# Performance work log

Measured on AMD Instinct MI355X. Metric: run time of the kernel, lower is better.

Reference implementation:

```python
import jax, jax.numpy as jnp
import numpy as np

K = 16      # n_sample neighbors
L = 2       # stacked PT blocks
D = 128     # in_dim
H = 128     # hidden_dim = out_dim = vector_dim
EPS = 1e-5


def _bn(x, g, b, axes):
    # batch-norm with batch statistics (train-mode MinkowskiBatchNorm / BN1d / BN2d)
    m = jnp.mean(x, axes, keepdims=True)
    v = jnp.var(x, axes, keepdims=True)
    return (x - m) * jax.lax.rsqrt(v + EPS) * g + b


def setup_inputs():
    key = jax.random.key(0)
    ks = jax.random.split(key, 16)
    B, Nper = 2, 8192
    coords = jax.random.randint(ks[0], (B, Nper, 3), 0, 200, dtype=jnp.int32)
    feats = jax.random.normal(ks[1], (B * Nper, D), dtype=jnp.float32)
    w = lambda k, s: jax.random.normal(k, s, dtype=jnp.float32) * 0.1
    return {
        'coords': coords, 'feats': feats,
        'W_top': w(ks[2], (L, D, H)),
        'bn_top_g': jnp.ones((L, H)), 'bn_top_b': jnp.zeros((L, H)),
        'W_phi': w(ks[3], (L, H, H)),
        'W_psi': w(ks[4], (L, H, H)),
        'W_alpha': w(ks[5], (L, H, H)),
        'W_d1': w(ks[6], (L, 3, H)), 'b_d1': jnp.zeros((L, H)),
        'bn_d1_g': jnp.ones((L, H)), 'bn_d1_b': jnp.zeros((L, H)),
        'W_d2': w(ks[7], (L, H, H)), 'b_d2': jnp.zeros((L, H)),
        'bn_d2_g': jnp.ones((L, H)), 'bn_d2_b': jnp.zeros((L, H)),
        'W_g1': w(ks[8], (L, H, H)), 'b_g1': jnp.zeros((L, H)),
        'bn_g1_g': jnp.ones((L, H)), 'bn_g1_b': jnp.zeros((L, H)),
        'W_g2': w(ks[9], (L, H, H)), 'b_g2': jnp.zeros((L, H)),
        'bn_g2_g': jnp.ones((L, H)), 'bn_g2_b': jnp.zeros((L, H)),
        'W_down': w(ks[10], (L, H, D)),
        'bn_down_g': jnp.ones((L, D)), 'bn_down_b': jnp.zeros((L, D)),
    }


def _knn(coords):
    # cube_query with USE_KNN=True: per-scene KNN grouping (self included)
    cf = coords.astype(jnp.float32)

    def one(c):  # c: (Nper, 3)
        d2 = jnp.sum((c[:, None, :] - c[None, :, :]) ** 2, -1)  # (Nper, Nper)
        _, idx = jax.lax.top_k(-d2, K)
        return idx

    idx = jax.vmap(one)(cf)                      # (B, Nper, K) per-scene indices
    nbr = jax.vmap(lambda c, i: c[i])(cf, idx)   # (B, Nper, K, 3) grouped coords
    rel = nbr - cf[:, :, None, :]                # relative xyz (pose input)
    B, Nper = coords.shape[0], coords.shape[1]
    gidx = (idx + (jnp.arange(B, dtype=idx.dtype) * Nper)[:, None, None]).reshape(-1, K)
    return rel.reshape(-1, K, 3), gidx           # (N,K,3), (N,K) global indices


def reference(coords, feats, W_top, bn_top_g, bn_top_b, W_phi, W_psi, W_alpha,
              W_d1, b_d1, bn_d1_g, bn_d1_b, W_d2, b_d2, bn_d2_g, bn_d2_b,
              W_g1, b_g1, bn_g1_g, bn_g1_b, W_g2, b_g2, bn_g2_g, bn_g2_b,
              W_down, bn_down_g, bn_down_b):
    rel, gidx = _knn(coords)
    f = feats
    for l in range(L):
        h = _bn(f @ W_top[l], bn_top_g[l], bn_top_b[l], 0)  # linear_top (1x1 conv + BN)
        # delta: pointwise MLP 3 -> H -> H on relative xyz (position encoding)
        pose = jax.nn.relu(_bn(rel @ W_d1[l] + b_d1[l], bn_d1_g[l], bn_d1_b[l], (0, 1)))
        pose = _bn(pose @ W_d2[l] + b_d2[l], bn_d2_g[l], bn_d2_b[l], (0, 1))  # (N,K,H)
        q = h @ W_phi[l]               # (N, H)
        kk = (h @ W_psi[l])[gidx]      # neighbor keys   (N, K, H)
        v = (h @ W_alpha[l])[gidx]     # neighbor values (N, K, H)
        # gamma: pointwise MLP on (phi - psi + pose), vector attention logits
        a = q[:, None, :] - kk + pose
        a = jax.nn.relu(_bn(a @ W_g1[l] + b_g1[l], bn_g1_g[l], bn_g1_b[l], (0, 1)))
        a = _bn(a @ W_g2[l] + b_g2[l], bn_g2_g[l], bn_g2_b[l], (0, 1))
        attn = jax.nn.softmax(a, axis=1)          # per-channel softmax over K neighbors
        y = jnp.sum(attn * (v + pose), axis=1)    # (N, H) vector-attention aggregation
        y = _bn(y @ W_down[l], bn_down_g[l], bn_down_b[l], 0)  # linear_down + BN
        f = y + f                                  # residual
    return f
```

## Files before the change

### kernel.cpp

```cpp
#include <hip/hip_runtime.h>

using u16 = unsigned short;
using u32 = unsigned int;
using u64 = unsigned long long;

#define NPTS   16384
#define NPER   8192
#define KNN    16
#define NKROWS (NPTS*KNN)
#define HD     128
#define CAP    208
#define NSLOT  16
#define NREG   10

typedef _Float16 half8 __attribute__((ext_vector_type(8)));
typedef float    floatx4 __attribute__((ext_vector_type(4)));
typedef short          s16x2 __attribute__((ext_vector_type(2)));
typedef unsigned short u16x2 __attribute__((ext_vector_type(2)));
typedef _Float16       h2v   __attribute__((ext_vector_type(2)));

__device__ __forceinline__ u16  f2h(float f){ _Float16 h=(_Float16)f; return __builtin_bit_cast(u16,h); }
__device__ __forceinline__ float h2f(u16 u){ return (float)__builtin_bit_cast(_Float16,u); }
__device__ __forceinline__ u32 umin32(u32 a,u32 b){ return a<b?a:b; }
__device__ __forceinline__ u32 mbcnt64(u64 m){
    return __builtin_amdgcn_mbcnt_hi((u32)(m>>32), __builtin_amdgcn_mbcnt_lo((u32)m,0));
}
__device__ __forceinline__ h2v bch2(u32 x){ return __builtin_bit_cast(h2v,x); }
__device__ __forceinline__ u32 bcu(h2v x){ return __builtin_bit_cast(u32,x); }
__device__ __forceinline__ u32 pk_relu(u32 x){
    u32 r;
    asm("v_pk_max_f16 %0, %1, %2" : "=v"(r) : "v"(x), "v"(0u));
    return r;
}
__device__ __forceinline__ int sdot2_acc(s16x2 a, int c){
#if __has_builtin(__builtin_amdgcn_sdot2)
    return __builtin_amdgcn_sdot2(a, a, c, false);
#else
    return (int)a.x*(int)a.x + (int)a.y*(int)a.y + c;
#endif
}

__global__ __launch_bounds__(256) void pack_coords(const int* __restrict__ coords, u32* __restrict__ pc){
    int i = blockIdx.x*256 + threadIdx.x;
    pc[i] = (u32)coords[3*i] | ((u32)coords[3*i+1]<<8) | ((u32)coords[3*i+2]<<16);
}

struct WPtrs { const float* p[8]; };
__global__ __launch_bounds__(256) void prep_weights(WPtrs wp, u16* __restrict__ wt){
    int idx = blockIdx.x*256 + threadIdx.x;
    int t = idx>>15, rem = idx&32767;
    int l = rem>>14, e = rem&16383;
    int n = e>>7, k = e&127;
    wt[idx] = f2h(wp.p[t][l*16384 + k*128 + n]);
}

__global__ __launch_bounds__(512) void knn3(const u32* __restrict__ pc, int* __restrict__ idx_g,
                                            float* __restrict__ rel, u64* __restrict__ sM){
    __shared__ u32 sc[NPER];
    __shared__ u32 buf[8][CAP];
    __shared__ u64 red[9];
    int tid = threadIdx.x;
    int wave = tid>>6, lane = tid&63;
    int scene = blockIdx.x >> 10;
    int q = (blockIdx.x & 1023)*8 + wave;

    const uint4* s4 = (const uint4*)(pc + scene*NPER);
#pragma unroll
    for (int i=0;i<4;i++) ((uint4*)sc)[tid + i*512] = s4[tid + i*512];
    if (tid<9) red[tid]=0;
    if (lane<16) buf[wave][lane]=0xFFFFFFFFu;
    __syncthreads();

    u32 qp = sc[q];
    int qx=(int)(qp&255), qy=(int)((qp>>8)&255), qz=(int)((qp>>16)&255);
    s16x2 qxy = __builtin_bit_cast(s16x2, __builtin_amdgcn_perm(0u, qp, 0x04010400u));
    s16x2 qzz = __builtin_bit_cast(s16x2, (qp>>16) * 0x00010001u);
    u32 thresh = 0xFFFFFFFFu;
    u32 td2 = thresh >> 13;
    u32 cnt = 16;

    auto tighten = [&](){
        u32 v0 = (lane      < (int)cnt) ? buf[wave][lane]      : 0xFFFFFFFFu;
        u32 v1 = (lane+64   < (int)cnt) ? buf[wave][lane+64]   : 0xFFFFFFFFu;
        u32 v2 = (lane+128  < (int)cnt) ? buf[wave][lane+128]  : 0xFFFFFFFFu;
        u32 v3 = (lane+192  < (int)cnt) ? buf[wave][lane+192]  : 0xFFFFFFFFu;
        u32 T = 0;
#pragma unroll
        for (int b=29;b>=0;b--){
            u32 Tt = T | (1u<<b);
            int c = __popcll(__ballot(v0<Tt)) + __popcll(__ballot(v1<Tt))
                  + __popcll(__ballot(v2<Tt)) + __popcll(__ballot(v3<Tt));
            if (c < 16) T = Tt;
        }
        u64 m0=__ballot(v0<=T), m1=__ballot(v1<=T), m2=__ballot(v2<=T), m3=__ballot(v3<=T);
        u32 b0=(u32)__popcll(m0), b1=(u32)__popcll(m1), b2=(u32)__popcll(m2);
        if (v0<=T) buf[wave][mbcnt64(m0)]=v0;
        if (v1<=T) buf[wave][b0+mbcnt64(m1)]=v1;
        if (v2<=T) buf[wave][b0+b1+mbcnt64(m2)]=v2;
        if (v3<=T) buf[wave][b0+b1+b2+mbcnt64(m3)]=v3;
        cnt = 16;
        thresh = T;
        td2 = T >> 13;
    };

    int lane2 = lane*2;
    uint2 p2 = ((const uint2*)sc)[lane];
    for (int t=0;t<64;t++){
        uint2 cur = p2;
        if (t<63) p2 = ((const uint2*)sc)[(t+1)*64+lane];
        u32 pa = cur.x, pb = cur.y;
        s16x2 xy0 = __builtin_bit_cast(s16x2, __builtin_amdgcn_perm(0u, pa, 0x04010400u));
        s16x2 xy1 = __builtin_bit_cast(s16x2, __builtin_amdgcn_perm(0u, pb, 0x04010400u));
        u32 zzr = __builtin_amdgcn_perm(pb, pa, 0x00060002u) & 0x00FF00FFu;
        s16x2 dzz = __builtin_bit_cast(s16x2, zzr) - qzz;
        u16x2 dzu = __builtin_bit_cast(u16x2, dzz);
        u16x2 zsq = dzu*dzu;
        u32 zb = __builtin_bit_cast(u32, zsq);
        s16x2 dxy0 = xy0 - qxy;
        s16x2 dxy1 = xy1 - qxy;
        u32 d2_0 = (u32)sdot2_acc(dxy0, (int)(zb & 0xFFFFu));
        u32 d2_1 = (u32)sdot2_acc(dxy1, (int)(zb >> 16));
        u64 m0 = __ballot(d2_0 <= td2);
        if (m0){
            int base = t*128 + lane2;
            if (d2_0 <= td2) buf[wave][cnt + mbcnt64(m0)] = (d2_0<<13) + (u32)base;
            cnt += (u32)__popcll(m0);
            if (cnt > CAP-64) tighten();
        }
        u64 m1 = __ballot(d2_1 <= td2);
        if (m1){
            int base = t*128 + lane2;
            if (d2_1 <= td2) buf[wave][cnt + mbcnt64(m1)] = (d2_1<<13) + (u32)(base+1);
            cnt += (u32)__popcll(m1);
            if (cnt > CAP-64) tighten();
        }
    }
    tighten();

    {
        u32 myk = buf[wave][lane & 15];
        u32 rank = 0;
#pragma unroll
        for (int j=0;j<16;j++){ u32 o = buf[wave][j]; rank += (o < myk) ? 1u : 0u; }
        if (lane < 16) buf[wave][rank] = myk;
    }

    int n = scene*NPER + q;
    u32 key = buf[wave][lane & 15];
    int dx=0,dy=0,dz=0;
    if (lane<16){
        int j = (int)(key & 8191u);
        idx_g[(size_t)n*KNN + lane] = scene*NPER + j;
        u32 p = sc[j];
        dx=(int)(p&255)-qx; dy=(int)((p>>8)&255)-qy; dz=(int)((p>>16)&255)-qz;
        size_t ro = ((size_t)n*KNN+lane)*3;
        rel[ro]=(float)dx; rel[ro+1]=(float)dy; rel[ro+2]=(float)dz;
    }
    int arr[9] = {dx,dy,dz, dx*dx,dy*dy,dz*dz, dx*dy,dx*dz,dy*dz};
#pragma unroll
    for (int o=32;o>=1;o>>=1)
#pragma unroll
        for (int j=0;j<9;j++) arr[j] += __shfl_xor(arr[j], o, 64);
    if (lane==0)
#pragma unroll
        for (int j=0;j<9;j++) atomicAdd(&red[j], (u64)(long long)arr[j]);
    __syncthreads();
    if (tid<9) atomicAdd(&sM[tid], red[tid]);
}

__global__ __launch_bounds__(256) void finalize_d1(const u64* __restrict__ sM, const float* __restrict__ W_d1,
        const float* __restrict__ b_d1, const float* __restrict__ g, const float* __restrict__ beta,
        float* __restrict__ A, float* __restrict__ C){
    int tid=threadIdx.x; int l=tid>>7, c=tid&127;
    double s0=(double)(long long)sM[0], s1=(double)(long long)sM[1], s2=(double)(long long)sM[2];
    double m00=(double)(long long)sM[3], m11=(double)(long long)sM[4], m22=(double)(long long)sM[5];
    double m01=(double)(long long)sM[6], m02=(double)(long long)sM[7], m12=(double)(long long)sM[8];
    double w0=W_d1[l*384+c], w1=W_d1[l*384+128+c], w2=W_d1[l*384+256+c];
    double b =b_d1[l*128+c];
    double S = s0*w0+s1*w1+s2*w2;
    double Q = m00*w0*w0+m11*w1*w1+m22*w2*w2 + 2.0*(m01*w0*w1+m02*w0*w2+m12*w1*w2);
    double cnt = (double)NKROWS;
    double mean = S/cnt + b;
    double ex2  = (Q + 2.0*b*S)/cnt + b*b;
    double var  = ex2 - mean*mean;
    float a = g[l*128+c] * (float)(1.0/sqrt(var+1e-5));
    A[l*128+c]=a; C[l*128+c]=beta[l*128+c]-(float)mean*a;
}

__device__ __forceinline__ void affine_reduce(const double* __restrict__ Pin,
        const float* __restrict__ gin, const float* __restrict__ bin, double cntD,
        float* Ash, float* Csh, int c){
    double s=0.0, q=0.0;
#pragma unroll
    for (int k=0;k<NSLOT;k++){ s+=Pin[k*256+c]; q+=Pin[k*256+128+c]; }
    double mean=s/cntD, var=q/cntD-mean*mean;
    float a = gin[c] * (float)(1.0/sqrt(var+1e-5));
    Ash[c]=a; Csh[c]=bin[c]-(float)mean*a;
}

struct CompF32 {
    const float* src;
    __device__ __forceinline__ void stage(u16* As,int R0,int k0,int tid,
            const float*,const float*,const _Float16*,const _Float16*) const {
#pragma unroll
        for (int u=0;u<8;u++){
            int flat=u*256+tid, row=flat>>4, c4=flat&15; int k=k0+c4*4;
            const float4 v=*(const float4*)(src+(size_t)(R0+row)*HD+k);
            ushort4 o; o.x=f2h(v.x); o.y=f2h(v.y); o.z=f2h(v.z); o.w=f2h(v.w);
            *(ushort4*)(As+row*72+c4*4)=o;
        }
    }
};
struct CompH16Aff {
    const u16* src;
    __device__ __forceinline__ void stage(u16* As,int R0,int k0,int tid,
            const float* Aa,const float* Ca,const _Float16*,const _Float16*) const {
#pragma unroll
        for (int u=0;u<8;u++){
            int flat=u*256+tid, row=flat>>4, c4=flat&15; int k=k0+c4*4;
            const ushort4 v=*(const ushort4*)(src+(size_t)(R0+row)*HD+k);
            ushort4 o;
            o.x=f2h(h2f(v.x)*Aa[k]  +Ca[k]);   o.y=f2h(h2f(v.y)*Aa[k+1]+Ca[k+1]);
            o.z=f2h(h2f(v.z)*Aa[k+2]+Ca[k+2]); o.w=f2h(h2f(v.w)*Aa[k+3]+Ca[k+3]);
            *(ushort4*)(As+row*72+c4*4)=o;
        }
    }
};
struct CompH16AffRelu {
    const u16* src;
    __device__ __forceinline__ void stage(u16* As,int R0,int k0,int tid,
            const float*,const float*,const _Float16* Ah,const _Float16* Ch) const {
#pragma unroll
        for (int u=0;u<8;u++){
            int flat=u*256+tid, row=flat>>4, c4=flat&15; int k=k0+c4*4;
            const uint2 v=*(const uint2*)(src+(size_t)(R0+row)*HD+k);
            h2v A0=*(const h2v*)(Ah+k), A1=*(const h2v*)(Ah+k+2);
            h2v C0=*(const h2v*)(Ch+k), C1=*(const h2v*)(Ch+k+2);
            uint2 o;
            o.x = pk_relu(bcu(bch2(v.x)*A0 + C0));
            o.y = pk_relu(bcu(bch2(v.y)*A1 + C1));
            *(uint2*)(As+row*72+c4*4)=o;
        }
    }
};
struct CompPose1 {
    const float* rel; const float* Wd1; const float* bd1; const float* Aa; const float* Ca;
    __device__ __forceinline__ void stage(u16* As,int R0,int k0,int tid,
            const float*,const float*,const _Float16*,const _Float16*) const {
#pragma unroll
        for (int u=0;u<8;u++){
            int flat=u*256+tid, row=flat>>4, c4=flat&15; int k=k0+c4*4; int R=R0+row;
            float r0=rel[(size_t)R*3], r1=rel[(size_t)R*3+1], r2=rel[(size_t)R*3+2];
            ushort4 o;
#pragma unroll
            for (int j=0;j<4;j++){
                int kk=k+j;
                float x = r0*Wd1[kk] + r1*Wd1[HD+kk] + r2*Wd1[2*HD+kk] + bd1[kk];
                x = fmaxf(x*Aa[kk]+Ca[kk], 0.f);
                ((u16*)&o)[j]=f2h(x);
            }
            *(ushort4*)(As+row*72+c4*4)=o;
        }
    }
};
struct CompA0 {
    const u16* q; const u16* kp; const u16* pose; const int* gidx;
    __device__ __forceinline__ void stage(u16* As,int R0,int k0,int tid,
            const float*,const float*,const _Float16* Ah,const _Float16* Ch) const {
#pragma unroll
        for (int u=0;u<8;u++){
            int flat=u*256+tid, row=flat>>4, c4=flat&15; int k=k0+c4*4; int R=R0+row;
            int n=R>>4; int g=gidx[R];
            const uint2 qv=*(const uint2*)(q +(size_t)n*HD+k);
            const uint2 kv=*(const uint2*)(kp+(size_t)g*HD+k);
            const uint2 pv=*(const uint2*)(pose+(size_t)R*HD+k);
            h2v A0=*(const h2v*)(Ah+k), A1=*(const h2v*)(Ah+k+2);
            h2v C0=*(const h2v*)(Ch+k), C1=*(const h2v*)(Ch+k+2);
            uint2 o;
            o.x = bcu(bch2(qv.x) - bch2(kv.x) + (bch2(pv.x)*A0 + C0));
            o.y = bcu(bch2(qv.y) - bch2(kv.y) + (bch2(pv.y)*A1 + C1));
            *(uint2*)(As+row*72+c4*4)=o;
        }
    }
};

template<class Comp, bool OUT16, bool HASBIAS, bool STATS, bool AFF>
__global__ __launch_bounds__(256) void gemm128(Comp comp, const u16* __restrict__ Wt,
        const float* __restrict__ bias, void* __restrict__ outp, double* __restrict__ statsP,
        int wtStride, long outStride,
        const double* __restrict__ Pin, const float* __restrict__ gin,
        const float* __restrict__ bin, double cntD){
    __shared__ __align__(16) u16 As[128*72];
    __shared__ __align__(16) u16 Bs[128*72];
    __shared__ float cs2[2][128], cq2[2][128];
    __shared__ float Aaff[128], Caff[128];
    __shared__ _Float16 Ah16[128], Ch16[128];
    const u16* W = Wt + (size_t)blockIdx.y*wtStride;
    u16*   o16 = (u16*)outp   + (size_t)blockIdx.y*outStride;
    float* o32 = (float*)outp + (size_t)blockIdx.y*outStride;
    int tid=threadIdx.x;
    if (AFF){
        if (tid<128){
            affine_reduce(Pin, gin, bin, cntD, Aaff, Caff, tid);
            Ah16[tid]=(_Float16)Aaff[tid]; Ch16[tid]=(_Float16)Caff[tid];
        }
        __syncthreads();
    }
    int R0=blockIdx.x*128;
    int lane=tid&63, wave=tid>>6, quad=lane>>4, r16=lane&15;
    int wm=wave>>1, wn=wave&1;
    floatx4 acc[4][4]={};
#pragma unroll
    for (int ks=0;ks<2;ks++){
        int k0=ks*64;
        comp.stage(As,R0,k0,tid,Aaff,Caff,Ah16,Ch16);
#pragma unroll
        for (int u=0;u<4;u++){
            int flat=u*256+tid, n=flat>>3, c8=flat&7;
            *(int4*)(Bs+n*72+c8*8) = *(const int4*)(W+n*HD+k0+c8*8);
        }
        __syncthreads();
#pragma unroll
        for (int kk2=0;kk2<2;kk2++){
            half8 aF[4], bF[4];
#pragma unroll
            for (int mi=0;mi<4;mi++) aF[mi]=*(const half8*)(As+(wm*64+mi*16+r16)*72 + kk2*32+quad*8);
#pragma unroll
            for (int ni=0;ni<4;ni++) bF[ni]=*(const half8*)(Bs+(wn*64+ni*16+r16)*72 + kk2*32+quad*8);
#pragma unroll
            for (int mi=0;mi<4;mi++)
#pragma unroll
                for (int ni=0;ni<4;ni++)
                    acc[mi][ni]=__builtin_amdgcn_mfma_f32_16x16x32_f16(aF[mi],bF[ni],acc[mi][ni],0,0,0);
        }
        __syncthreads();
    }
    float sAcc[4]={0,0,0,0}, qAcc[4]={0,0,0,0};
#pragma unroll
    for (int mi=0;mi<4;mi++)
#pragma unroll
        for (int ni=0;ni<4;ni++){
            int col=wn*64+ni*16+r16;
            float bv = HASBIAS ? bias[col] : 0.f;
#pragma unroll
            for (int rg=0;rg<4;rg++){
                int row=R0+wm*64+mi*16+quad*4+rg;
                float v=acc[mi][ni][rg]+bv;
                if (STATS){ sAcc[ni]+=v; qAcc[ni]+=v*v; }
                if (OUT16) o16[(size_t)row*HD+col]=f2h(v);
                else       o32[(size_t)row*HD+col]=v;
            }
        }
    if (STATS){
#pragma unroll
        for (int ni=0;ni<4;ni++){
            float s=sAcc[ni], q=qAcc[ni];
            s += __shfl_xor(s,16,64); s += __shfl_xor(s,32,64);
            q += __shfl_xor(q,16,64); q += __shfl_xor(q,32,64);
            if (quad==0){
                int col=wn*64+ni*16+r16;
                cs2[wm][col]=s; cq2[wm][col]=q;
            }
        }
        __syncthreads();
        if (tid<128){
            int slot = blockIdx.x & (NSLOT-1);
            unsafeAtomicAdd(&statsP[slot*256+tid],     (double)(cs2[0][tid]+cs2[1][tid]));
            unsafeAtomicAdd(&statsP[slot*256+128+tid], (double)(cq2[0][tid]+cq2[1][tid]));
        }
    }
}

__global__ __launch_bounds__(256) void aggregate(const u16* __restrict__ a2, const u16* __restrict__ pose,
        const u16* __restrict__ vv, const int* __restrict__ gidx,
        const double* __restrict__ Pg2, const float* __restrict__ g_g2, const float* __restrict__ b_g2,
        const double* __restrict__ Pd2, const float* __restrict__ g_d2, const float* __restrict__ b_d2,
        float* __restrict__ y){
    __shared__ float Ag2s[128], Cg2s[128], Ad2s[128], Cd2s[128];
    int t=threadIdx.x;
    {
        int cc=t&127;
        const double* Pp = (t<128)? Pg2 : Pd2;
        const float*  gg = (t<128)? g_g2 : g_d2;
        const float*  bb = (t<128)? b_g2 : b_d2;
        float* Adst = (t<128)? Ag2s : Ad2s;
        float* Cdst = (t<128)? Cg2s : Cd2s;
        affine_reduce(Pp, gg, bb, (double)NKROWS, Adst, Cdst, cc);
    }
    __syncthreads();
    int c=(t&63)*2, h=t>>6;
    int n=blockIdx.x*4+h;
    float sA0=Ag2s[c], sC0=Cg2s[c], pA0=Ad2s[c], pC0=Cd2s[c];
    float sA1=Ag2s[c+1], sC1=Cg2s[c+1], pA1=Ad2s[c+1], pC1=Cd2s[c+1];
    float av0[16], av1[16]; float m0=-1e30f, m1=-1e30f;
#pragma unroll
    for (int k=0;k<16;k++){
        ushort2 tt=*(const ushort2*)(a2+((size_t)n*16+k)*HD+c);
        float a0=h2f(tt.x)*sA0+sC0, a1=h2f(tt.y)*sA1+sC1;
        av0[k]=a0; av1[k]=a1; m0=fmaxf(m0,a0); m1=fmaxf(m1,a1);
    }
    float sum0=0.f, sum1=0.f;
#pragma unroll
    for (int k=0;k<16;k++){
        float e0=__expf(av0[k]-m0), e1=__expf(av1[k]-m1);
        av0[k]=e0; av1[k]=e1; sum0+=e0; sum1+=e1;
    }
    float acc0=0.f, acc1=0.f;
#pragma unroll
    for (int k=0;k<16;k++){
        int g=gidx[n*16+k];
        ushort2 pt=*(const ushort2*)(pose+((size_t)n*16+k)*HD+c);
        ushort2 vt=*(const ushort2*)(vv+(size_t)g*HD+c);
        acc0 += av0[k]*(h2f(pt.x)*pA0+pC0 + h2f(vt.x));
        acc1 += av1[k]*(h2f(pt.y)*pA1+pC1 + h2f(vt.y));
    }
    y[(size_t)n*HD+c]  =acc0/sum0;
    y[(size_t)n*HD+c+1]=acc1/sum1;
}

__global__ __launch_bounds__(256) void residual(const float* __restrict__ ydown,
        const double* __restrict__ Pin, const float* __restrict__ gin, const float* __restrict__ bin,
        const float* __restrict__ fin, float* __restrict__ fout){
    __shared__ float Ash[128], Csh[128];
    int tid=threadIdx.x;
    if (tid<128) affine_reduce(Pin, gin, bin, (double)NPTS, Ash, Csh, tid);
    __syncthreads();
    size_t i=((size_t)blockIdx.x*256+tid)*4; int c=(int)(i&127);
    float4 yv=*(const float4*)(ydown+i);
    float4 fv=*(const float4*)(fin+i);
    float4 o;
    o.x=yv.x*Ash[c]  +Csh[c]  +fv.x;
    o.y=yv.y*Ash[c+1]+Csh[c+1]+fv.y;
    o.z=yv.z*Ash[c+2]+Csh[c+2]+fv.z;
    o.w=yv.w*Ash[c+3]+Csh[c+3]+fv.w;
    *(float4*)(fout+i)=o;
}

extern "C" void kernel_launch(void* const* d_in, const int* in_sizes, int n_in,
                              void* d_out, int out_size, void* d_ws, size_t ws_size,
                              hipStream_t stream){
    const int*   coords=(const int*)d_in[0];
    const float* feats=(const float*)d_in[1];
    const float* W_top=(const float*)d_in[2];
    const float* g_top=(const float*)d_in[3];
    const float* bt_top=(const float*)d_in[4];
    const float* W_phi=(const float*)d_in[5];
    const float* W_psi=(const float*)d_in[6];
    const float* W_alp=(const float*)d_in[7];
    const float* W_d1=(const float*)d_in[8];
    const float* b_d1=(const float*)d_in[9];
    const float* g_d1=(const float*)d_in[10];
    const float* bt_d1=(const float*)d_in[11];
    const float* W_d2=(const float*)d_in[12];
    const float* b_d2=(const float*)d_in[13];
    const float* g_d2=(const float*)d_in[14];
    const float* bt_d2=(const float*)d_in[15];
    const float* W_g1=(const float*)d_in[16];
    const float* b_g1=(const float*)d_in[17];
    const float* g_g1=(const float*)d_in[18];
    const float* bt_g1=(const float*)d_in[19];
    const float* W_g2=(const float*)d_in[20];
    const float* b_g2=(const float*)d_in[21];
    const float* g_g2=(const float*)d_in[22];
    const float* bt_g2=(const float*)d_in[23];
    const float* W_dn=(const float*)d_in[24];
    const float* g_dn=(const float*)d_in[25];
    const float* bt_dn=(const float*)d_in[26];

    char* ws=(char*)d_ws;
    size_t off=0;
    auto carve=[&](size_t bytes)->char*{ char* p=ws+off; off=(off+bytes+255)&~(size_t)255; return p; };
    u32*    pc    =(u32*)   carve((size_t)NPTS*4);
    int*    idxg  =(int*)   carve((size_t)NKROWS*4);
    float*  rel   =(float*) carve((size_t)NKROWS*3*4);
    u16*    h16   =(u16*)   carve((size_t)NPTS*HD*2);
    u16*    qb    =(u16*)   carve((size_t)3*NPTS*HD*2);
    u16*    kpb   = qb + (size_t)NPTS*HD;
    u16*    vvb   = qb + (size_t)2*NPTS*HD;
    float*  yb    =(float*) carve((size_t)NPTS*HD*4);
    float*  ydown =(float*) carve((size_t)NPTS*HD*4);
    float*  fbuf  =(float*) carve((size_t)NPTS*HD*4);
    u16*    wt    =(u16*)   carve((size_t)8*2*16384*2);
    char*   stats =         carve((size_t)NREG*NSLOT*256*8 + 256);
    double* P     =(double*)stats;
    u64*    sM    =(u64*)(stats + (size_t)NREG*NSLOT*256*8);
    float*  aff   =(float*) carve(4096);
    float *A_d1=aff, *C_d1=aff+256;
    u16*    pose2 =(u16*)   carve((size_t)NKROWS*HD*2);
    u16*    abuf  =(u16*)   carve((size_t)NKROWS*HD*2);
    if (ws_size < off) return;

    auto Preg=[&](int stage,int l)->double*{ return P + (size_t)(stage*2+l)*(NSLOT*256); };

    hipMemsetAsync(stats, 0, (size_t)NREG*NSLOT*256*8 + 256, stream);
    pack_coords<<<dim3(NPTS/256),dim3(256),0,stream>>>(coords, pc);
    WPtrs wp{{W_top,W_phi,W_psi,W_alp,W_d2,W_g1,W_g2,W_dn}};
    prep_weights<<<dim3(8*2*16384/256),dim3(256),0,stream>>>(wp, wt);
    knn3<<<dim3(2048),dim3(512),0,stream>>>(pc, idxg, rel, sM);
    finalize_d1<<<dim3(1),dim3(256),0,stream>>>(sM, W_d1, b_d1, g_d1, bt_d1, A_d1, C_d1);

    const float* fin=feats;
    for (int l=0;l<2;l++){
        const u16* wt_top=wt+(0*2+l)*16384; const u16* wt_phi=wt+(1*2+l)*16384;
        const u16* wt_d2 =wt+(4*2+l)*16384; const u16* wt_g1 =wt+(5*2+l)*16384;
        const u16* wt_g2 =wt+(6*2+l)*16384; const u16* wt_dn =wt+(7*2+l)*16384;

        gemm128<CompF32,true,false,true,false><<<dim3(NPTS/128),dim3(256),0,stream>>>(
            CompF32{fin}, wt_top, nullptr, h16, Preg(0,l), 0, 0, nullptr, nullptr, nullptr, 0.0);

        gemm128<CompH16Aff,true,false,false,true><<<dim3(NPTS/128,3),dim3(256),0,stream>>>(
            CompH16Aff{h16}, wt_phi, nullptr, qb, nullptr, 2*16384, (long)NPTS*HD,
            Preg(0,l), g_top+l*128, bt_top+l*128, (double)NPTS);

        gemm128<CompPose1,true,true,true,false><<<dim3(NKROWS/128),dim3(256),0,stream>>>(
            CompPose1{rel, W_d1+l*384, b_d1+l*128, A_d1+l*128, C_d1+l*128}, wt_d2, b_d2+l*128, pose2,
            Preg(1,l), 0, 0, nullptr, nullptr, nullptr, 0.0);

        gemm128<CompA0,true,true,true,true><<<dim3(NKROWS/128),dim3(256),0,stream>>>(
            CompA0{qb,kpb,pose2,idxg}, wt_g1, b_g1+l*128, abuf, Preg(2,l), 0, 0,
            Preg(1,l), g_d2+l*128, bt_d2+l*128, (double)NKROWS);

        gemm128<CompH16AffRelu,true,true,true,true><<<dim3(NKROWS/128),dim3(256),0,stream>>>(
            CompH16AffRelu{abuf}, wt_g2, b_g2+l*128, abuf, Preg(3,l), 0, 0,
            Preg(2,l), g_g1+l*128, bt_g1+l*128, (double)NKROWS);

        aggregate<<<dim3(NPTS/4),dim3(256),0,stream>>>(abuf, pose2, vvb, idxg,
            Preg(3,l), g_g2+l*128, bt_g2+l*128, Preg(1,l), g_d2+l*128, bt_d2+l*128, yb);

        gemm128<CompF32,false,false,true,false><<<dim3(NPTS/128),dim3(256),0,stream>>>(
            CompF32{yb}, wt_dn, nullptr, ydown, Preg(4,l), 0, 0, nullptr, nullptr, nullptr, 0.0);
        residual<<<dim3(NPTS*HD/1024),dim3(256),0,stream>>>(ydown,
            Preg(4,l), g_dn+l*128, bt_dn+l*128, fin, (l==1)?(float*)d_out:fbuf);
        fin=fbuf;
    }
}
```

Measured before the change: 515.3 us.

## Load GEMM A-fragments directly from global memory, stage full weight tile once

The GEMM kernel no longer stages the A operand (the activation tile, computed on the fly with affine/relu/gather) through LDS. Each lane now loads and transforms its own MFMA fragment straight from global memory into registers. The whole 128x128 weight matrix is staged into LDS once with a wider padded stride, which removes the per-k-step barriers, and launch bounds now request 4 blocks per SM. The aim is to cut LDS traffic and synchronization and to raise occupancy. The cost is that each wave re-reads A rows in a less coalesced 16-byte-per-lane pattern, and the two waves sharing the same rows both do the transform and the loads.

Result: slower. 874.6 us (+69.7%).

```diff
diff --git a/kernel.cpp b/kernel.cpp
--- a/kernel.cpp
+++ b/kernel.cpp
@@ -12,6 +12,7 @@
 #define CAP    208
 #define NSLOT  16
 #define NREG   10
+#define BSTR   136
 
 typedef _Float16 half8 __attribute__((ext_vector_type(8)));
 typedef float    floatx4 __attribute__((ext_vector_type(4)));
@@ -200,98 +201,114 @@
 
 struct CompF32 {
     const float* src;
-    __device__ __forceinline__ void stage(u16* As,int R0,int k0,int tid,
-            const float*,const float*,const _Float16*,const _Float16*) const {
-#pragma unroll
-        for (int u=0;u<8;u++){
-            int flat=u*256+tid, row=flat>>4, c4=flat&15; int k=k0+c4*4;
-            const float4 v=*(const float4*)(src+(size_t)(R0+row)*HD+k);
-            ushort4 o; o.x=f2h(v.x); o.y=f2h(v.y); o.z=f2h(v.z); o.w=f2h(v.w);
-            *(ushort4*)(As+row*72+c4*4)=o;
+    __device__ __forceinline__ void frags(half8* aF, int rbase, int kb,
+            const float*, const float*, const _Float16*, const _Float16*) const {
+#pragma unroll
+        for (int mi=0;mi<4;mi++){
+            const float* p = src + (size_t)(rbase+mi*16)*HD + kb;
+            float4 v0 = *(const float4*)p;
+            float4 v1 = *(const float4*)(p+4);
+            half8 r;
+            r[0]=(_Float16)v0.x; r[1]=(_Float16)v0.y; r[2]=(_Float16)v0.z; r[3]=(_Float16)v0.w;
+            r[4]=(_Float16)v1.x; r[5]=(_Float16)v1.y; r[6]=(_Float16)v1.z; r[7]=(_Float16)v1.w;
+            aF[mi]=r;
         }
     }
 };
 struct CompH16Aff {
     const u16* src;
-    __device__ __forceinline__ void stage(u16* As,int R0,int k0,int tid,
-            const float* Aa,const float* Ca,const _Float16*,const _Float16*) const {
-#pragma unroll
-        for (int u=0;u<8;u++){
-            int flat=u*256+tid, row=flat>>4, c4=flat&15; int k=k0+c4*4;
-            const ushort4 v=*(const ushort4*)(src+(size_t)(R0+row)*HD+k);
-            ushort4 o;
-            o.x=f2h(h2f(v.x)*Aa[k]  +Ca[k]);   o.y=f2h(h2f(v.y)*Aa[k+1]+Ca[k+1]);
-            o.z=f2h(h2f(v.z)*Aa[k+2]+Ca[k+2]); o.w=f2h(h2f(v.w)*Aa[k+3]+Ca[k+3]);
-            *(ushort4*)(As+row*72+c4*4)=o;
+    __device__ __forceinline__ void frags(half8* aF, int rbase, int kb,
+            const float* Aa, const float* Ca, const _Float16*, const _Float16*) const {
+        float a0=Aa[kb],a1=Aa[kb+1],a2=Aa[kb+2],a3=Aa[kb+3],a4=Aa[kb+4],a5=Aa[kb+5],a6=Aa[kb+6],a7=Aa[kb+7];
+        float c0=Ca[kb],c1=Ca[kb+1],c2=Ca[kb+2],c3=Ca[kb+3],c4=Ca[kb+4],c5=Ca[kb+5],c6=Ca[kb+6],c7=Ca[kb+7];
+#pragma unroll
+        for (int mi=0;mi<4;mi++){
+            const u16* p = src + (size_t)(rbase+mi*16)*HD + kb;
+            ushort4 u0 = *(const ushort4*)p;
+            ushort4 u1 = *(const ushort4*)(p+4);
+            half8 r;
+            r[0]=(_Float16)(h2f(u0.x)*a0+c0); r[1]=(_Float16)(h2f(u0.y)*a1+c1);
+            r[2]=(_Float16)(h2f(u0.z)*a2+c2); r[3]=(_Float16)(h2f(u0.w)*a3+c3);
+            r[4]=(_Float16)(h2f(u1.x)*a4+c4); r[5]=(_Float16)(h2f(u1.y)*a5+c5);
+            r[6]=(_Float16)(h2f(u1.z)*a6+c6); r[7]=(_Float16)(h2f(u1.w)*a7+c7);
+            aF[mi]=r;
         }
     }
 };
 struct CompH16AffRelu {
     const u16* src;
-    __device__ __forceinline__ void stage(u16* As,int R0,int k0,int tid,
-            const float*,const float*,const _Float16* Ah,const _Float16* Ch) const {
-#pragma unroll
-        for (int u=0;u<8;u++){
-            int flat=u*256+tid, row=flat>>4, c4=flat&15; int k=k0+c4*4;
-            const uint2 v=*(const uint2*)(src+(size_t)(R0+row)*HD+k);
-            h2v A0=*(const h2v*)(Ah+k), A1=*(const h2v*)(Ah+k+2);
-            h2v C0=*(const h2v*)(Ch+k), C1=*(const h2v*)(Ch+k+2);
-            uint2 o;
+    __device__ __forceinline__ void frags(half8* aF, int rbase, int kb,
+            const float*, const float*, const _Float16* Ah, const _Float16* Ch) const {
+        h2v A0=*(const h2v*)(Ah+kb), A1=*(const h2v*)(Ah+kb+2), A2=*(const h2v*)(Ah+kb+4), A3=*(const h2v*)(Ah+kb+6);
+        h2v C0=*(const h2v*)(Ch+kb), C1=*(const h2v*)(Ch+kb+2), C2=*(const h2v*)(Ch+kb+4), C3=*(const h2v*)(Ch+kb+6);
+#pragma unroll
+        for (int mi=0;mi<4;mi++){
+            uint4 v = *(const uint4*)(src + (size_t)(rbase+mi*16)*HD + kb);
+            uint4 o;
             o.x = pk_relu(bcu(bch2(v.x)*A0 + C0));
             o.y = pk_relu(bcu(bch2(v.y)*A1 + C1));
-            *(uint2*)(As+row*72+c4*4)=o;
+            o.z = pk_relu(bcu(bch2(v.z)*A2 + C2));
+            o.w = pk_relu(bcu(bch2(v.w)*A3 + C3));
+            aF[mi]=__builtin_bit_cast(half8,o);
         }
     }
 };
 struct CompPose1 {
     const float* rel; const float* Wd1; const float* bd1; const float* Aa; const float* Ca;
-    __device__ __forceinline__ void stage(u16* As,int R0,int k0,int tid,
-            const float*,const float*,const _Float16*,const _Float16*) const {
-#pragma unroll
-        for (int u=0;u<8;u++){
-            int flat=u*256+tid, row=flat>>4, c4=flat&15; int k=k0+c4*4; int R=R0+row;
+    __device__ __forceinline__ void frags(half8* aF, int rbase, int kb,
+            const float*, const float*, const _Float16*, const _Float16*) const {
+        float w0[8],w1[8],w2[8],bb[8],av[8],cv[8];
+#pragma unroll
+        for (int j=0;j<8;j++){
+            int col=kb+j;
+            w0[j]=Wd1[col]; w1[j]=Wd1[HD+col]; w2[j]=Wd1[2*HD+col];
+            bb[j]=bd1[col]; av[j]=Aa[col]; cv[j]=Ca[col];
+        }
+#pragma unroll
+        for (int mi=0;mi<4;mi++){
+            int R=rbase+mi*16;
             float r0=rel[(size_t)R*3], r1=rel[(size_t)R*3+1], r2=rel[(size_t)R*3+2];
-            ushort4 o;
-#pragma unroll
-            for (int j=0;j<4;j++){
-                int kk=k+j;
-                float x = r0*Wd1[kk] + r1*Wd1[HD+kk] + r2*Wd1[2*HD+kk] + bd1[kk];
-                x = fmaxf(x*Aa[kk]+Ca[kk], 0.f);
-                ((u16*)&o)[j]=f2h(x);
+            half8 r;
+#pragma unroll
+            for (int j=0;j<8;j++){
+                float x = r0*w0[j] + r1*w1[j] + r2*w2[j] + bb[j];
+                x = fmaxf(x*av[j]+cv[j], 0.f);
+                r[j]=(_Float16)x;
             }
-            *(ushort4*)(As+row*72+c4*4)=o;
+            aF[mi]=r;
         }
     }
 };
 struct CompA0 {
     const u16* q; const u16* kp; const u16* pose; const int* gidx;
-    __device__ __forceinline__ void stage(u16* As,int R0,int k0,int tid,
-            const float*,const float*,const _Float16* Ah,const _Float16* Ch) const {
-#pragma unroll
-        for (int u=0;u<8;u++){
-            int flat=u*256+tid, row=flat>>4, c4=flat&15; int k=k0+c4*4; int R=R0+row;
+    __device__ __forceinline__ void frags(half8* aF, int rbase, int kb,
+            const float*, const float*, const _Float16* Ah, const _Float16* Ch) const {
+        h2v A0=*(const h2v*)(Ah+kb), A1=*(const h2v*)(Ah+kb+2), A2=*(const h2v*)(Ah+kb+4), A3=*(const h2v*)(Ah+kb+6);
+        h2v C0=*(const h2v*)(Ch+kb), C1=*(const h2v*)(Ch+kb+2), C2=*(const h2v*)(Ch+kb+4), C3=*(const h2v*)(Ch+kb+6);
+#pragma unroll
+        for (int mi=0;mi<4;mi++){
+            int R=rbase+mi*16;
             int n=R>>4; int g=gidx[R];
-            const uint2 qv=*(const uint2*)(q +(size_t)n*HD+k);
-            const uint2 kv=*(const uint2*)(kp+(size_t)g*HD+k);
-            const uint2 pv=*(const uint2*)(pose+(size_t)R*HD+k);
-            h2v A0=*(const h2v*)(Ah+k), A1=*(const h2v*)(Ah+k+2);
-            h2v C0=*(const h2v*)(Ch+k), C1=*(const h2v*)(Ch+k+2);
-            uint2 o;
+            uint4 qv = *(const uint4*)(q   +(size_t)n*HD+kb);
+            uint4 kv = *(const uint4*)(kp  +(size_t)g*HD+kb);
+            uint4 pv = *(const uint4*)(pose+(size_t)R*HD+kb);
+            uint4 o;
             o.x = bcu(bch2(qv.x) - bch2(kv.x) + (bch2(pv.x)*A0 + C0));
             o.y = bcu(bch2(qv.y) - bch2(kv.y) + (bch2(pv.y)*A1 + C1));
-            *(uint2*)(As+row*72+c4*4)=o;
+            o.z = bcu(bch2(qv.z) - bch2(kv.z) + (bch2(pv.z)*A2 + C2));
+            o.w = bcu(bch2(qv.w) - bch2(kv.w) + (bch2(pv.w)*A3 + C3));
+            aF[mi]=__builtin_bit_cast(half8,o);
         }
     }
 };
 
 template<class Comp, bool OUT16, bool HASBIAS, bool STATS, bool AFF>
-__global__ __launch_bounds__(256) void gemm128(Comp comp, const u16* __restrict__ Wt,
+__global__ __launch_bounds__(256,4) void gemm128(Comp comp, const u16* __restrict__ Wt,
         const float* __restrict__ bias, void* __restrict__ outp, double* __restrict__ statsP,
         int wtStride, long outStride,
         const double* __restrict__ Pin, const float* __restrict__ gin,
         const float* __restrict__ bin, double cntD){
-    __shared__ __align__(16) u16 As[128*72];
-    __shared__ __align__(16) u16 Bs[128*72];
+    __shared__ __align__(16) u16 Bs[128*BSTR];
     __shared__ float cs2[2][128], cq2[2][128];
     __shared__ float Aaff[128], Caff[128];
     __shared__ _Float16 Ah16[128], Ch16[128];
@@ -304,36 +321,33 @@
             affine_reduce(Pin, gin, bin, cntD, Aaff, Caff, tid);
             Ah16[tid]=(_Float16)Aaff[tid]; Ch16[tid]=(_Float16)Caff[tid];
         }
-        __syncthreads();
-    }
+    }
+#pragma unroll
+    for (int u=0;u<8;u++){
+        int flat=u*256+tid, n=flat>>4, c=flat&15;
+        *(int4*)(Bs + n*BSTR + c*8) = *(const int4*)(W + n*HD + c*8);
+    }
+    __syncthreads();
+
     int R0=blockIdx.x*128;
     int lane=tid&63, wave=tid>>6, quad=lane>>4, r16=lane&15;
     int wm=wave>>1, wn=wave&1;
+    int rbase = R0 + wm*64 + r16;
     floatx4 acc[4][4]={};
 #pragma unroll
-    for (int ks=0;ks<2;ks++){
-        int k0=ks*64;
-        comp.stage(As,R0,k0,tid,Aaff,Caff,Ah16,Ch16);
-#pragma unroll
-        for (int u=0;u<4;u++){
-            int flat=u*256+tid, n=flat>>3, c8=flat&7;
-            *(int4*)(Bs+n*72+c8*8) = *(const int4*)(W+n*HD+k0+c8*8);
-        }
-        __syncthreads();
-#pragma unroll
-        for (int kk2=0;kk2<2;kk2++){
-            half8 aF[4], bF[4];
-#pragma unroll
-            for (int mi=0;mi<4;mi++) aF[mi]=*(const half8*)(As+(wm*64+mi*16+r16)*72 + kk2*32+quad*8);
-#pragma unroll
-            for (int ni=0;ni<4;ni++) bF[ni]=*(const half8*)(Bs+(wn*64+ni*16+r16)*72 + kk2*32+quad*8);
-#pragma unroll
-            for (int mi=0;mi<4;mi++)
-#pragma unroll
-                for (int ni=0;ni<4;ni++)
-                    acc[mi][ni]=__builtin_amdgcn_mfma_f32_16x16x32_f16(aF[mi],bF[ni],acc[mi][ni],0,0,0);
-        }
-        __syncthreads();
+    for (int ks=0;ks<2;ks++)
+#pragma unroll
+    for (int kk2=0;kk2<2;kk2++){
+        int kb = ks*64 + kk2*32 + quad*8;
+        half8 aF[4], bF[4];
+        comp.frags(aF, rbase, kb, Aaff, Caff, Ah16, Ch16);
+#pragma unroll
+        for (int ni=0;ni<4;ni++) bF[ni]=*(const half8*)(Bs+(size_t)(wn*64+ni*16+r16)*BSTR+kb);
+#pragma unroll
+        for (int mi=0;mi<4;mi++)
+#pragma unroll
+            for (int ni=0;ni<4;ni++)
+                acc[mi][ni]=__builtin_amdgcn_mfma_f32_16x16x32_f16(aF[mi],bF[ni],acc[mi][ni],0,0,0);
     }
     float sAcc[4]={0,0,0,0}, qAcc[4]={0,0,0,0};
 #pragma unroll
```
